# Optimization experiments

Hardware: AMD Instinct MI355X
Metric: run time of the kernel (lower is better)

Reference implementation:

```python
import jax, jax.numpy as jnp
import numpy as np

OUTPUT_SIZE = 7


def _make_bbox(key, n, hw):
    k1, k2, k3, k4 = jax.random.split(key, 4)
    maxc = float(hw - 1)
    x1 = jax.random.uniform(k1, (n,)) * (maxc * 0.5)
    y1 = jax.random.uniform(k2, (n,)) * (maxc * 0.5)
    x2 = jnp.minimum(x1 + 4.0 + jax.random.uniform(k3, (n,)) * (maxc * 0.5), maxc)
    y2 = jnp.minimum(y1 + 4.0 + jax.random.uniform(k4, (n,)) * (maxc * 0.5), maxc)
    return jnp.stack([x1, y1, x2, y2], axis=1).astype(jnp.float32)


def setup_inputs() -> dict:
    key = jax.random.key(0)
    kf, kb = jax.random.split(key)
    N, C, H, W = 512, 256, 32, 32
    feature = jax.random.normal(kf, (N, C, H, W), dtype=jnp.float32)
    bbox = _make_bbox(kb, N, H)
    return {"feature": feature, "bbox": bbox}


def _bilinear_sample(feature, xs, ys):
    # feature: [N,C,H,W]; xs, ys: [N,G] continuous sample coordinates.
    N, C, H, W = feature.shape
    G = xs.shape[1]
    x0 = jnp.clip(jnp.floor(xs), 0, W - 1)
    y0 = jnp.clip(jnp.floor(ys), 0, H - 1)
    x0i = x0.astype(jnp.int32)
    y0i = y0.astype(jnp.int32)
    x1i = jnp.minimum(x0i + 1, W - 1)
    y1i = jnp.minimum(y0i + 1, H - 1)
    wx = (xs - x0)[:, None, :]   # [N,1,G] weight along x for grid [N,G_y,G_x]
    wy = (ys - y0)[:, :, None]   # [N,G,1]

    n_idx = jnp.arange(N)[:, None, None]          # [N,1,1]
    yj0 = y0i[:, :, None]                          # [N,G,1]
    yj1 = y1i[:, :, None]
    xi0 = x0i[:, None, :]                          # [N,1,G]
    xi1 = x1i[:, None, :]

    # advanced indexing -> [N,G,G,C], then move C forward
    v00 = feature[n_idx, :, yj0, xi0]
    v01 = feature[n_idx, :, yj0, xi1]
    v10 = feature[n_idx, :, yj1, xi0]
    v11 = feature[n_idx, :, yj1, xi1]

    wxe = wx[:, :, :, None]  # broadcast over channel (last) axis
    wye = wy[:, :, :, None]
    sampled = ((1 - wye) * ((1 - wxe) * v00 + wxe * v01)
               + wye * ((1 - wxe) * v10 + wxe * v11))  # [N,G,G,C]
    return jnp.transpose(sampled, (0, 3, 1, 2))  # [N,C,G,G]


def reference(feature, bbox):
    N, C, H, W = feature.shape
    S = OUTPUT_SIZE
    G = 2 * S
    x_steps = (bbox[:, 2] - bbox[:, 0]) / G  # [N]
    y_steps = (bbox[:, 3] - bbox[:, 1]) / G
    g = jnp.arange(G, dtype=feature.dtype)   # [G]
    xs = bbox[:, 0:1] + g[None, :] * x_steps[:, None]  # [N,G]
    ys = bbox[:, 1:2] + g[None, :] * y_steps[:, None]  # [N,G]
    sampled = _bilinear_sample(feature, xs, ys)        # [N,C,G,G]
    # 2x2 max pool, stride 2 -> [N,C,S,S]
    pooled = sampled.reshape(N, C, S, 2, S, 2).max(axis=(3, 5))
    return pooled
```

## Files before the change

### kernel.cpp

```cpp
#include <hip/hip_runtime.h>
#include <math.h>

#define CH 8
#define RMAX 22

__global__ __launch_bounds__(256, 7) void roialign_kernel(
    const float* __restrict__ feat, const float* __restrict__ bbox,
    float* __restrict__ out) {
  __shared__ float lds[CH * RMAX * 32];
  __shared__ int   sxg0[14], sxl0[14], sxg1[14], sxl1[14];
  __shared__ int   sy0r[14], sy1r[14];
  __shared__ float swx[14], swy[14];

  const int blk = blockIdx.x;
  const int n  = blk >> 5;
  const int c0 = (blk & 31) * CH;
  const int t  = threadIdx.x;

  const float bx1 = bbox[n * 4 + 0];
  const float by1 = bbox[n * 4 + 1];
  const float bx2 = bbox[n * 4 + 2];
  const float by2 = bbox[n * 4 + 3];
  const float xstep = (bx2 - bx1) * (1.0f / 14.0f);
  const float ystep = (by2 - by1) * (1.0f / 14.0f);

  const int ylo = min(max((int)floorf(by1), 0), 31);
  const float ys13 = by1 + 13.0f * ystep;
  int yhi = min(min(max((int)floorf(ys13), 0), 31) + 1, 31);
  yhi = min(yhi, ylo + (RMAX - 1));
  const int perch = (yhi - ylo + 1) * 8;

  if (t < 14) {
    float xs = bx1 + (float)t * xstep;
    float x0 = fminf(fmaxf(floorf(xs), 0.0f), 31.0f);
    int x0i = (int)x0;
    int x1i = min(x0i + 1, 31);
    sxg0[t] = x0i >> 2;
    sxl0[t] = x0i & 3;
    sxg1[t] = x1i >> 2;
    sxl1[t] = x1i & 3;
    swx[t] = xs - x0;
  } else if (t < 28) {
    int g = t - 14;
    float yv = by1 + (float)g * ystep;
    float y0 = fminf(fmaxf(floorf(yv), 0.0f), 31.0f);
    int y0i = (int)y0;
    int y1i = min(y0i + 1, 31);
    y0i = min(max(y0i, ylo), yhi);
    y1i = min(max(y1i, ylo), yhi);
    sy0r[g] = y0i - ylo;
    sy1r[g] = y1i - ylo;
    swy[g] = yv - y0;
  }

  {
    const float4* __restrict__ src =
        (const float4*)(feat + (size_t)n * (256 * 1024));
    float4* dst = (float4*)lds;
    const int c    = t >> 5;
    const int lane = t & 31;
    const int cb   = c * (RMAX * 8);
    const size_t gb = (size_t)(c0 + c) * 256 + ylo * 8;
    for (int off = lane; off < perch; off += 32) {
      int yr = off >> 3;
      int q  = off & 7;
      int sq = (q + yr + c) & 7;
      dst[cb + yr * 8 + sq] = src[gb + off];
    }
  }
  __syncthreads();

  float* outp = out + ((size_t)n * 256 + c0) * 49;
  for (int o = t; o < CH * 49; o += 256) {
    int cl = o / 49;
    int s  = o - cl * 49;
    int sy = s / 7;
    int sx = s - sy * 7;
    const float* plane = lds + cl * (RMAX * 32);
    float m = -INFINITY;
#pragma unroll
    for (int i = 0; i < 2; ++i) {
      int   yr0 = sy0r[2 * sy + i];
      int   yr1 = sy1r[2 * sy + i];
      float wy  = swy[2 * sy + i];
      const float* r0 = plane + yr0 * 32;
      const float* r1 = plane + yr1 * 32;
      const int rot0 = yr0 + cl;
      const int rot1 = yr1 + cl;
#pragma unroll
      for (int j = 0; j < 2; ++j) {
        int   gx  = 2 * sx + j;
        int   xg0 = sxg0[gx], xl0 = sxl0[gx];
        int   xg1 = sxg1[gx], xl1 = sxl1[gx];
        float wx  = swx[gx];
        float v00 = r0[(((xg0 + rot0) & 7) << 2) + xl0];
        float v01 = r0[(((xg1 + rot0) & 7) << 2) + xl1];
        float v10 = r1[(((xg0 + rot1) & 7) << 2) + xl0];
        float v11 = r1[(((xg1 + rot1) & 7) << 2) + xl1];
        float top = fmaf(wx, v01 - v00, v00);
        float bot = fmaf(wx, v11 - v10, v10);
        float val = fmaf(wy, bot - top, top);
        m = fmaxf(m, val);
      }
    }
    outp[o] = m;
  }
}

extern "C" void kernel_launch(void* const* d_in, const int* in_sizes, int n_in,
                              void* d_out, int out_size, void* d_ws, size_t ws_size,
                              hipStream_t stream) {
  const float* feat = (const float*)d_in[0];
  const float* bbox = (const float*)d_in[1];
  float* out = (float*)d_out;
  dim3 grid(512 * (256 / CH));
  roialign_kernel<<<grid, 256, 0, stream>>>(feat, bbox, out);
}
```

Before: 45.84 us.

## Use direct global-to-LDS loads with one wave per channel and smaller blocks

Shrinks each block from 8 to 4 channels, so the grid doubles. Each wave now stages one channel's ROI rows straight into LDS with global_load_lds 16-byte transfers, which avoids the round trip through registers. The swizzle is applied on the global side so the existing rotated LDS indexing still works. Each wave then computes its channel's 49 outputs with a single pass, and occupancy is raised to 8 blocks per SIMD-group. The risk is that global_load_lds writes fixed lane-contiguous LDS slots and the permuted source addresses may produce less coalesced global reads. Also, only 49 of 64 lanes do useful compute.

```diff
diff --git a/kernel.cpp b/kernel.cpp
--- a/kernel.cpp
+++ b/kernel.cpp
@@ -1,21 +1,26 @@
 #include <hip/hip_runtime.h>
 #include <math.h>
 
-#define CH 8
-#define RMAX 22
+#define CH   4
+#define RPAD 24
 
-__global__ __launch_bounds__(256, 7) void roialign_kernel(
+typedef __attribute__((address_space(1))) const void gptr_t;
+typedef __attribute__((address_space(3))) void lptr_t;
+
+__global__ __launch_bounds__(256, 8) void roialign_kernel(
     const float* __restrict__ feat, const float* __restrict__ bbox,
     float* __restrict__ out) {
-  __shared__ float lds[CH * RMAX * 32];
+  __shared__ float lds[CH * RPAD * 32];
   __shared__ int   sxg0[14], sxl0[14], sxg1[14], sxl1[14];
   __shared__ int   sy0r[14], sy1r[14];
   __shared__ float swx[14], swy[14];
 
   const int blk = blockIdx.x;
-  const int n  = blk >> 5;
-  const int c0 = (blk & 31) * CH;
+  const int n  = blk >> 6;
+  const int c0 = (blk & 63) * CH;
   const int t  = threadIdx.x;
+  const int wv = t >> 6;
+  const int ln = t & 63;
 
   const float bx1 = bbox[n * 4 + 0];
   const float by1 = bbox[n * 4 + 1];
@@ -27,8 +32,8 @@
   const int ylo = min(max((int)floorf(by1), 0), 31);
   const float ys13 = by1 + 13.0f * ystep;
   int yhi = min(min(max((int)floorf(ys13), 0), 31) + 1, 31);
-  yhi = min(yhi, ylo + (RMAX - 1));
-  const int perch = (yhi - ylo + 1) * 8;
+  yhi = min(yhi, ylo + (RPAD - 1));
+  const int R = yhi - ylo + 1;
 
   if (t < 14) {
     float xs = bx1 + (float)t * xstep;
@@ -54,29 +59,27 @@
   }
 
   {
-    const float4* __restrict__ src =
-        (const float4*)(feat + (size_t)n * (256 * 1024));
-    float4* dst = (float4*)lds;
-    const int c    = t >> 5;
-    const int lane = t & 31;
-    const int cb   = c * (RMAX * 8);
-    const size_t gb = (size_t)(c0 + c) * 256 + ylo * 8;
-    for (int off = lane; off < perch; off += 32) {
-      int yr = off >> 3;
-      int q  = off & 7;
-      int sq = (q + yr + c) & 7;
-      dst[cb + yr * 8 + sq] = src[gb + off];
+    const float* srcbase =
+        feat + (size_t)n * (256 * 1024) + (size_t)(c0 + wv) * 1024;
+    float* dstbase = lds + wv * (RPAD * 32);
+    const int yr_l = ln >> 3;
+    const int q    = ln & 7;
+    for (int it = 0; it * 8 < R; ++it) {
+      int yr   = it * 8 + yr_l;
+      int srow = min(yr, R - 1);
+      int qp   = (q - yr - wv) & 7;
+      const float* gp = srcbase + (ylo + srow) * 32 + qp * 4;
+      lptr_t* lp = (lptr_t*)(dstbase + it * 256);
+      __builtin_amdgcn_global_load_lds((gptr_t*)gp, lp, 16, 0, 0);
     }
   }
+  asm volatile("s_waitcnt vmcnt(0)" ::: "memory");
   __syncthreads();
 
-  float* outp = out + ((size_t)n * 256 + c0) * 49;
-  for (int o = t; o < CH * 49; o += 256) {
-    int cl = o / 49;
-    int s  = o - cl * 49;
-    int sy = s / 7;
-    int sx = s - sy * 7;
-    const float* plane = lds + cl * (RMAX * 32);
+  if (ln < 49) {
+    const int sy = ln / 7;
+    const int sx = ln - sy * 7;
+    const float* plane = lds + wv * (RPAD * 32);
     float m = -INFINITY;
 #pragma unroll
     for (int i = 0; i < 2; ++i) {
@@ -85,8 +88,8 @@
       float wy  = swy[2 * sy + i];
       const float* r0 = plane + yr0 * 32;
       const float* r1 = plane + yr1 * 32;
-      const int rot0 = yr0 + cl;
-      const int rot1 = yr1 + cl;
+      const int rot0 = yr0 + wv;
+      const int rot1 = yr1 + wv;
 #pragma unroll
       for (int j = 0; j < 2; ++j) {
         int   gx  = 2 * sx + j;
@@ -103,7 +106,7 @@
         m = fmaxf(m, val);
       }
     }
-    outp[o] = m;
+    out[((size_t)n * 256 + c0 + wv) * 49 + ln] = m;
   }
 }
 
```

Result: no change. 45.40 us (-1.0%).
